# Performance work log

Hardware: AMD Instinct MI355X
Metric: run time of the kernel (lower is better)

Reference implementation:

```python
import jax, jax.numpy as jnp
import numpy as np

B, D, H, W = 32, 64, 64, 64
K = 1024

def setup_inputs() -> dict:
    key = jax.random.key(0)
    k1, k2 = jax.random.split(key)
    x = jax.random.normal(k1, (B, D, H, W), dtype=jnp.float32)
    # nn.Parameter(torch.rand(embeddings_dim, num_embeddings)) -> uniform [0,1)
    emb = jax.random.uniform(k2, (D, K), dtype=jnp.float32)
    return {"x": x, "emb": emb}


def reference(x, emb):
    # x: [B, D, H, W], emb: [D, K]
    b, d, h, w = x.shape
    xf = jnp.transpose(x, (0, 2, 3, 1)).reshape(-1, d)  # [N, D], N = B*H*W
    # squared L2 distance (same argmin as torch.norm(.,2) distance)
    d2 = (
        jnp.sum(xf * xf, axis=-1, keepdims=True)
        - 2.0 * (xf @ emb)
        + jnp.sum(emb * emb, axis=0)
    )  # [N, K]
    argmin = jnp.argmin(d2, axis=-1)  # [N]
    # gather codebook vectors: emb.T[argmin] -> [N, D]
    q = jnp.take(emb.T, argmin, axis=0)
    result = jnp.transpose(q.reshape(b, h, w, d), (0, 3, 1, 2))  # [B, D, H, W]
    return result, argmin.reshape(b, h, w)
```

## Files before the change

kernel.cpp:

```cpp
#include <hip/hip_runtime.h>


using half8 = __attribute__((ext_vector_type(8))) _Float16;
using half4 = __attribute__((ext_vector_type(4))) _Float16;
using f32x4 = __attribute__((ext_vector_type(4))) float;

#define XPITCH 72

__global__ void prep_kernel(const float* __restrict__ emb,
                            float* __restrict__ e2,
                            _Float16* __restrict__ eTh,
                            _Float16* __restrict__ eTl) {
    int k = blockIdx.x * 64 + threadIdx.x;
    float s = 0.f;
#pragma unroll
    for (int c = 0; c < 8; ++c) {
        half8 hv, lv;
#pragma unroll
        for (int j = 0; j < 8; ++j) {
            float v = emb[(c * 8 + j) * 1024 + k];
            s = fmaf(v, v, s);
            _Float16 h = (_Float16)v;
            hv[j] = h;
            lv[j] = (_Float16)(v - (float)h);
        }
        *(half8*)(eTh + k * 64 + c * 8) = hv;
        *(half8*)(eTl + k * 64 + c * 8) = lv;
    }
    e2[k] = s;
}

__launch_bounds__(256)
__global__ void vq_kernel(const float* __restrict__ x,
                          const _Float16* __restrict__ eTh,
                          const _Float16* __restrict__ eTl,
                          const float* __restrict__ e2,
                          const float* __restrict__ emb,
                          float* __restrict__ outq,
                          float* __restrict__ outidx) {
    __shared__ _Float16 sxh[64 * XPITCH];
    __shared__ _Float16 sxl[64 * XPITCH];
    __shared__ float rbest[256];
    __shared__ int   ridx[256];
    __shared__ int   samin[64];

    const int tx = threadIdx.x;
    const int n0 = blockIdx.x * 64;
    const int bb = n0 >> 12;
    const int hw = n0 & 4095;
    const float* xbase = x + bb * 262144 + hw;

    {
        const int p  = tx & 63;
        const int dg = (tx >> 6) << 2;
#pragma unroll
        for (int it = 0; it < 4; ++it) {
            int d0 = it * 16 + dg;
            float v0 = xbase[(d0 + 0) * 4096 + p];
            float v1 = xbase[(d0 + 1) * 4096 + p];
            float v2 = xbase[(d0 + 2) * 4096 + p];
            float v3 = xbase[(d0 + 3) * 4096 + p];
            _Float16 h0 = (_Float16)v0, h1 = (_Float16)v1,
                     h2 = (_Float16)v2, h3 = (_Float16)v3;
            half4 hv = {h0, h1, h2, h3};
            half4 lv = {(_Float16)(v0 - (float)h0), (_Float16)(v1 - (float)h1),
                        (_Float16)(v2 - (float)h2), (_Float16)(v3 - (float)h3)};
            *(half4*)(sxh + p * XPITCH + d0) = hv;
            *(half4*)(sxl + p * XPITCH + d0) = lv;
        }
    }
    __syncthreads();

    const int lane = tx & 63;
    const int w    = tx >> 6;
    const int r16  = lane & 15;
    const int q    = lane >> 4;

    half8 ah[4][2], al[4][2];
#pragma unroll
    for (int mt = 0; mt < 4; ++mt)
#pragma unroll
        for (int s = 0; s < 2; ++s) {
            ah[mt][s] = *(const half8*)(sxh + (mt * 16 + r16) * XPITCH + s * 32 + q * 8);
            al[mt][s] = *(const half8*)(sxl + (mt * 16 + r16) * XPITCH + s * 32 + q * 8);
        }
#pragma unroll
    for (int mt = 0; mt < 4; ++mt)
#pragma unroll
        for (int s = 0; s < 2; ++s) {
            asm volatile("" : "+v"(ah[mt][s]));
            asm volatile("" : "+v"(al[mt][s]));
        }

    float best[16];
    int   bestk[16];
#pragma unroll
    for (int i = 0; i < 16; ++i) { best[i] = 3.4e38f; bestk[i] = 0; }

    const int kw = w << 8;
    const _Float16* bhbase = eTh + (kw + r16) * 64 + q * 8;
    const _Float16* blbase = eTl + (kw + r16) * 64 + q * 8;
    const float*    e2base = e2 + kw + r16;

    half8 pbh0, pbh1, pbl0, pbl1; float pe2;
    half8 qbh0, qbh1, qbl0, qbl1; float qe2;

#define LOADSET(BH0, BH1, BL0, BL1, E2V, TT)                                  \
    {                                                                         \
        const int off_ = (TT) << 10;                \
        BH0 = *(const half8*)(bhbase + off_);                                 \
        BH1 = *(const half8*)(bhbase + off_ + 32);                            \
        BL0 = *(const half8*)(blbase + off_);                                 \
        BL1 = *(const half8*)(blbase + off_ + 32);                            \
        E2V = e2base[(TT) << 4];                                              \
    }

#define COMPUTE(BH0, BH1, BL0, BL1, E2V, TT)                                  \
    {                                                                         \
        const int klc_ = kw + ((TT) << 4) + r16;                              \
        _Pragma("unroll")                                                     \
        for (int mt = 0; mt < 4; ++mt) {                                      \
            f32x4 a = {0.f, 0.f, 0.f, 0.f};                                   \
            a = __builtin_amdgcn_mfma_f32_16x16x32_f16(al[mt][0], BL0, a, 0, 0, 0); \
            a = __builtin_amdgcn_mfma_f32_16x16x32_f16(al[mt][1], BL1, a, 0, 0, 0); \
            a = __builtin_amdgcn_mfma_f32_16x16x32_f16(al[mt][0], BH0, a, 0, 0, 0); \
            a = __builtin_amdgcn_mfma_f32_16x16x32_f16(al[mt][1], BH1, a, 0, 0, 0); \
            a = __builtin_amdgcn_mfma_f32_16x16x32_f16(ah[mt][0], BL0, a, 0, 0, 0); \
            a = __builtin_amdgcn_mfma_f32_16x16x32_f16(ah[mt][1], BL1, a, 0, 0, 0); \
            a = __builtin_amdgcn_mfma_f32_16x16x32_f16(ah[mt][0], BH0, a, 0, 0, 0); \
            a = __builtin_amdgcn_mfma_f32_16x16x32_f16(ah[mt][1], BH1, a, 0, 0, 0); \
            _Pragma("unroll")                                                 \
            for (int rr = 0; rr < 4; ++rr) {                                  \
                float dist_ = fmaf(-2.f, a[rr], E2V);                         \
                int i_ = mt * 4 + rr;                                         \
                if (dist_ < best[i_]) { best[i_] = dist_; bestk[i_] = klc_; } \
            }                                                                 \
        }                                                                     \
    }

    LOADSET(pbh0, pbh1, pbl0, pbl1, pe2, 0);
#pragma unroll 1
    for (int t = 0; t < 16; t += 2) {
        LOADSET(qbh0, qbh1, qbl0, qbl1, qe2, t + 1);
        COMPUTE(pbh0, pbh1, pbl0, pbl1, pe2, t);
        LOADSET(pbh0, pbh1, pbl0, pbl1, pe2, (t + 2) & 15);
        COMPUTE(qbh0, qbh1, qbl0, qbl1, qe2, t + 1);
    }

#pragma unroll
    for (int i = 0; i < 16; ++i) {
        float bv = best[i];
        int   bk = bestk[i];
#pragma unroll
        for (int m = 1; m < 16; m <<= 1) {
            float ov = __shfl_xor(bv, m, 64);
            int   ok = __shfl_xor(bk, m, 64);
            if (ov < bv || (ov == bv && ok < bk)) { bv = ov; bk = ok; }
        }
        best[i] = bv;
        bestk[i] = bk;
    }
    if (r16 == 0) {
#pragma unroll
        for (int mt = 0; mt < 4; ++mt)
#pragma unroll
            for (int rr = 0; rr < 4; ++rr) {
                int p = mt * 16 + q * 4 + rr;
                rbest[w * 64 + p] = best[mt * 4 + rr];
                ridx[w * 64 + p]  = bestk[mt * 4 + rr];
            }
    }
    __syncthreads();

    if (tx < 64) {
        float bv = rbest[tx];
        int   bk = ridx[tx];
#pragma unroll
        for (int g = 1; g < 4; ++g) {
            float v  = rbest[g * 64 + tx];
            int   kk = ridx[g * 64 + tx];
            if (v < bv || (v == bv && kk < bk)) { bv = v; bk = kk; }
        }
        samin[tx] = bk;
        outidx[n0 + tx] = (float)bk;
    }
    __syncthreads();

    const int p = tx & 63;
    const int drow = tx >> 6;
    const int amin = samin[p];
    float* obase = outq + bb * 262144 + hw + p;
#pragma unroll
    for (int it = 0; it < 16; ++it) {
        int d = (it << 2) + drow;
        obase[d * 4096] = emb[d * 1024 + amin];
    }
}

extern "C" void kernel_launch(void* const* d_in, const int* in_sizes, int n_in,
                              void* d_out, int out_size, void* d_ws, size_t ws_size,
                              hipStream_t stream) {
    const float* x   = (const float*)d_in[0];
    const float* emb = (const float*)d_in[1];
    float* outq   = (float*)d_out;
    float* outidx = outq + 8388608;

    float*    e2  = (float*)d_ws;
    _Float16* eTh = (_Float16*)((char*)d_ws + 4096);
    _Float16* eTl = (_Float16*)((char*)d_ws + 4096 + 131072);

    prep_kernel<<<16, 64, 0, stream>>>(emb, e2, eTh, eTl);
    vq_kernel<<<2048, 256, 0, stream>>>(x, eTh, eTl, e2, emb, outq, outidx);
}
```

Baseline: 160.9 us.

## Double rows per block to 128 and pack best-tile indices into nibbles

```diff
diff --git a/kernel.cpp b/kernel.cpp
--- a/kernel.cpp
+++ b/kernel.cpp
@@ -30,7 +30,7 @@
     e2[k] = s;
 }
 
-__launch_bounds__(256)
+__launch_bounds__(256, 2)
 __global__ void vq_kernel(const float* __restrict__ x,
                           const _Float16* __restrict__ eTh,
                           const _Float16* __restrict__ eTl,
@@ -38,24 +38,24 @@
                           const float* __restrict__ emb,
                           float* __restrict__ outq,
                           float* __restrict__ outidx) {
-    __shared__ _Float16 sxh[64 * XPITCH];
-    __shared__ _Float16 sxl[64 * XPITCH];
-    __shared__ float rbest[256];
-    __shared__ int   ridx[256];
-    __shared__ int   samin[64];
+    __shared__ _Float16 sxh[128 * XPITCH];
+    __shared__ _Float16 sxl[128 * XPITCH];
+    __shared__ float rbest[4 * 128];
+    __shared__ int   ridx[4 * 128];
+    __shared__ int   samin[128];
 
     const int tx = threadIdx.x;
-    const int n0 = blockIdx.x * 64;
+    const int n0 = blockIdx.x * 128;
     const int bb = n0 >> 12;
     const int hw = n0 & 4095;
     const float* xbase = x + bb * 262144 + hw;
 
     {
-        const int p  = tx & 63;
-        const int dg = (tx >> 6) << 2;
-#pragma unroll
-        for (int it = 0; it < 4; ++it) {
-            int d0 = it * 16 + dg;
+        const int p     = tx & 127;
+        const int dbase = (tx >> 7) << 5;
+#pragma unroll
+        for (int it = 0; it < 8; ++it) {
+            int d0 = dbase + it * 4;
             float v0 = xbase[(d0 + 0) * 4096 + p];
             float v1 = xbase[(d0 + 1) * 4096 + p];
             float v2 = xbase[(d0 + 2) * 4096 + p];
@@ -76,26 +76,20 @@
     const int r16  = lane & 15;
     const int q    = lane >> 4;
 
-    half8 ah[4][2], al[4][2];
-#pragma unroll
-    for (int mt = 0; mt < 4; ++mt)
+    half8 ah[8][2], al[8][2];
+#pragma unroll
+    for (int mt = 0; mt < 8; ++mt)
 #pragma unroll
         for (int s = 0; s < 2; ++s) {
             ah[mt][s] = *(const half8*)(sxh + (mt * 16 + r16) * XPITCH + s * 32 + q * 8);
             al[mt][s] = *(const half8*)(sxl + (mt * 16 + r16) * XPITCH + s * 32 + q * 8);
         }
-#pragma unroll
-    for (int mt = 0; mt < 4; ++mt)
-#pragma unroll
-        for (int s = 0; s < 2; ++s) {
-            asm volatile("" : "+v"(ah[mt][s]));
-            asm volatile("" : "+v"(al[mt][s]));
-        }
-
-    float best[16];
-    int   bestk[16];
-#pragma unroll
-    for (int i = 0; i < 16; ++i) { best[i] = 3.4e38f; bestk[i] = 0; }
+    asm volatile("" ::: "memory");
+
+    float best[32];
+    unsigned int bt[4] = {0u, 0u, 0u, 0u};
+#pragma unroll
+    for (int i = 0; i < 32; ++i) best[i] = 3.4e38f;
 
     const int kw = w << 8;
     const _Float16* bhbase = eTh + (kw + r16) * 64 + q * 8;
@@ -117,9 +111,8 @@
 
 #define COMPUTE(BH0, BH1, BL0, BL1, E2V, TT)                                  \
     {                                                                         \
-        const int klc_ = kw + ((TT) << 4) + r16;                              \
         _Pragma("unroll")                                                     \
-        for (int mt = 0; mt < 4; ++mt) {                                      \
+        for (int mt = 0; mt < 8; ++mt) {                                      \
             f32x4 a = {0.f, 0.f, 0.f, 0.f};                                   \
             a = __builtin_amdgcn_mfma_f32_16x16x32_f16(al[mt][0], BL0, a, 0, 0, 0); \
             a = __builtin_amdgcn_mfma_f32_16x16x32_f16(al[mt][1], BL1, a, 0, 0, 0); \
@@ -132,8 +125,13 @@
             _Pragma("unroll")                                                 \
             for (int rr = 0; rr < 4; ++rr) {                                  \
                 float dist_ = fmaf(-2.f, a[rr], E2V);                         \
-                int i_ = mt * 4 + rr;                                         \
-                if (dist_ < best[i_]) { best[i_] = dist_; bestk[i_] = klc_; } \
+                const int i_ = mt * 4 + rr;                                   \
+                const int sh_ = (i_ & 7) * 4;                                 \
+                if (dist_ < best[i_]) {                                       \
+                    best[i_] = dist_;                                         \
+                    bt[i_ >> 3] = (bt[i_ >> 3] & ~(0xFu << sh_)) |            \
+                                  ((unsigned int)(TT) << sh_);                \
+                }                                                             \
             }                                                                 \
         }                                                                     \
     }
@@ -148,37 +146,33 @@
     }
 
 #pragma unroll
-    for (int i = 0; i < 16; ++i) {
-        float bv = best[i];
-        int   bk = bestk[i];
-#pragma unroll
-        for (int m = 1; m < 16; m <<= 1) {
-            float ov = __shfl_xor(bv, m, 64);
-            int   ok = __shfl_xor(bk, m, 64);
-            if (ov < bv || (ov == bv && ok < bk)) { bv = ov; bk = ok; }
-        }
-        best[i] = bv;
-        bestk[i] = bk;
-    }
-    if (r16 == 0) {
-#pragma unroll
-        for (int mt = 0; mt < 4; ++mt)
-#pragma unroll
-            for (int rr = 0; rr < 4; ++rr) {
-                int p = mt * 16 + q * 4 + rr;
-                rbest[w * 64 + p] = best[mt * 4 + rr];
-                ridx[w * 64 + p]  = bestk[mt * 4 + rr];
+    for (int mt = 0; mt < 8; ++mt)
+#pragma unroll
+        for (int rr = 0; rr < 4; ++rr) {
+            const int i = mt * 4 + rr;
+            float bv = best[i];
+            int   bk = kw + (int)(((bt[i >> 3] >> ((i & 7) * 4)) & 15u) << 4) + r16;
+#pragma unroll
+            for (int m = 1; m < 16; m <<= 1) {
+                float ov = __shfl_xor(bv, m, 64);
+                int   ok = __shfl_xor(bk, m, 64);
+                if (ov < bv || (ov == bv && ok < bk)) { bv = ov; bk = ok; }
             }
-    }
+            if (r16 == 0) {
+                const int p = mt * 16 + q * 4 + rr;
+                rbest[w * 128 + p] = bv;
+                ridx[w * 128 + p]  = bk;
+            }
+        }
     __syncthreads();
 
-    if (tx < 64) {
+    if (tx < 128) {
         float bv = rbest[tx];
         int   bk = ridx[tx];
 #pragma unroll
         for (int g = 1; g < 4; ++g) {
-            float v  = rbest[g * 64 + tx];
-            int   kk = ridx[g * 64 + tx];
+            float v  = rbest[g * 128 + tx];
+            int   kk = ridx[g * 128 + tx];
             if (v < bv || (v == bv && kk < bk)) { bv = v; bk = kk; }
         }
         samin[tx] = bk;
@@ -186,13 +180,13 @@
     }
     __syncthreads();
 
-    const int p = tx & 63;
-    const int drow = tx >> 6;
+    const int p = tx & 127;
+    const int drow = tx >> 7;
     const int amin = samin[p];
     float* obase = outq + bb * 262144 + hw + p;
 #pragma unroll
-    for (int it = 0; it < 16; ++it) {
-        int d = (it << 2) + drow;
+    for (int it = 0; it < 32; ++it) {
+        int d = (it << 1) + drow;
         obase[d * 4096] = emb[d * 1024 + amin];
     }
 }
@@ -210,5 +204,5 @@
     _Float16* eTl = (_Float16*)((char*)d_ws + 4096 + 131072);
 
     prep_kernel<<<16, 64, 0, stream>>>(emb, e2, eTh, eTl);
-    vq_kernel<<<2048, 256, 0, stream>>>(x, eTh, eTl, e2, emb, outq, outidx);
+    vq_kernel<<<1024, 256, 0, stream>>>(x, eTh, eTl, e2, emb, outq, outidx);
 }
```

New measurement: 162.5 us. No clear change (+1.0%).
